# Kernel tuning notes

Measured on AMD Instinct MI355X. Metric: run time of the kernel, lower is better.

Reference implementation:

```python
import jax, jax.numpy as jnp
import numpy as np

D = 1024   # input_size / width
H = 1024   # hidden_size / lru_width
TW = 4     # conv1d temporal width (Griffin default)
C_GATE = 8.0


def setup_inputs() -> dict:
    key = jax.random.key(0)
    ks = jax.random.split(key, 12)
    B, T = 8, 4096
    sd = 1.0 / np.sqrt(D)
    sh = 1.0 / np.sqrt(H)
    return {
        "input_bxtxd": jax.random.normal(ks[0], (B, T, D), jnp.float32),
        "w_x": jax.random.normal(ks[1], (D, H), jnp.float32) * sd,
        "b_x": jnp.zeros((H,), jnp.float32),
        "w_y": jax.random.normal(ks[2], (D, H), jnp.float32) * sd,
        "b_y": jnp.zeros((H,), jnp.float32),
        "conv_w": jax.random.normal(ks[3], (TW, H), jnp.float32) * 0.5,
        "conv_b": jnp.zeros((H,), jnp.float32),
        "gi_w": jax.random.normal(ks[4], (H, H), jnp.float32) * sh,
        "gi_b": jnp.zeros((H,), jnp.float32),
        "ga_w": jax.random.normal(ks[5], (H, H), jnp.float32) * sh,
        "ga_b": jnp.zeros((H,), jnp.float32),
        # a_param > 0 so a = exp(-c*gate*softplus(a_param)) lies in (0,1)
        "a_param": jax.random.uniform(ks[6], (H,), jnp.float32, 2.0, 6.0),
    }


def reference(input_bxtxd, w_x, b_x, w_y, b_y, conv_w, conv_b,
              gi_w, gi_b, ga_w, ga_b, a_param):
    x = input_bxtxd                      # [B,T,D], batch_first
    B, T, _ = x.shape

    # x branch: linear_x -> causal depthwise conv1d (zero cache) -> RG-LRU
    x1 = jnp.einsum("btd,dh->bth", x, w_x) + b_x            # [B,T,H]
    xp = jnp.pad(x1, ((0, 0), (TW - 1, 0), (0, 0)))          # causal pad
    x2 = sum(conv_w[i] * xp[:, i:i + T, :] for i in range(TW)) + conv_b

    # RG-LRU gates (num_heads=1 -> full linear)
    gate_x = jax.nn.sigmoid(jnp.einsum("bth,hk->btk", x2, gi_w) + gi_b)
    gate_a = jax.nn.sigmoid(jnp.einsum("bth,hk->btk", x2, ga_w) + ga_b)
    log_a = -C_GATE * gate_a * jax.nn.softplus(a_param)      # [B,T,H]
    a = jnp.exp(log_a)
    multiplier = jnp.sqrt(jnp.maximum(1.0 - jnp.exp(2.0 * log_a), 0.0))
    # segment_pos = arange(T): reset at t == 0
    multiplier = multiplier.at[:, 0, :].set(1.0)
    a = a.at[:, 0, :].set(0.0)
    normalized_x = gate_x * x2 * multiplier                  # [B,T,H]

    # linear recurrence h_t = a_t * h_{t-1} + normalized_x_t (h_{-1}=0)
    def combine(c1, c2):
        a1, h1 = c1
        a2, h2 = c2
        return a1 * a2, h2 + a2 * h1

    _, h = jax.lax.associative_scan(combine, (a, normalized_x), axis=1)

    # y branch and output gating
    y = jax.nn.gelu(jnp.einsum("btd,dh->bth", x, w_y) + b_y, approximate=False)
    out = h * y                                              # [B,T,H]
    hn = h[:, -1, :]                                         # last state
    return out, h, hn
```

## Files before the change

### kernel.cpp

```cpp
#include <hip/hip_runtime.h>
#include <math.h>


#define B_ 8
#define T_ 4096
#define H_ 1024
#define M_ (B_ * T_)
#define NC_ 128
#define CL_ 32

typedef _Float16 half8 __attribute__((ext_vector_type(8)));
typedef _Float16 half4 __attribute__((ext_vector_type(4)));
typedef float    f32x4 __attribute__((ext_vector_type(4)));

#define FENCE asm volatile("" ::: "memory")
#define BAR() do { FENCE; __builtin_amdgcn_s_barrier(); FENCE; } while (0)
#define MFMA16(a, b, c) __builtin_amdgcn_mfma_f32_16x16x32_f16((a), (b), (c), 0, 0, 0)

__device__ __forceinline__ void load16_lds(const _Float16* g, _Float16* l) {
  __builtin_amdgcn_global_load_lds(
      (const __attribute__((address_space(1))) void*)g,
      (__attribute__((address_space(3))) void*)l, 16, 0, 0);
}

__global__ __launch_bounds__(256) void transpose_cvt(
    const float* __restrict__ sA, const float* __restrict__ sB,
    _Float16* __restrict__ dst) {
  __shared__ float tile[32][33];
  int bn = blockIdx.x * 32;
  int bk = blockIdx.y * 32;
  const float* src = (bn < 1024) ? sA : sB;
  int nof = (bn < 1024) ? bn : bn - 1024;
  int c  = threadIdx.x & 31;
  int r0 = threadIdx.x >> 5;
#pragma unroll
  for (int i = 0; i < 4; ++i) {
    int r = r0 + i * 8;
    tile[r][c] = src[(size_t)(bk + r) * 1024 + nof + c];
  }
  __syncthreads();
#pragma unroll
  for (int i = 0; i < 4; ++i) {
    int nl = r0 + i * 8;
    dst[(size_t)(bn + nl) * 1024 + bk + c] = (_Float16)tile[c][nl];
  }
}

__global__ void prep_bias(const float* __restrict__ bx, const float* __restrict__ by,
                          const float* __restrict__ gib, const float* __restrict__ gab,
                          float* __restrict__ b1, float* __restrict__ b2) {
  int i = blockIdx.x * 1024 + threadIdx.x;
  if (i < 1024)      b1[i] = bx[i];
  else if (i < 2048) b1[i] = by[i - 1024];
  else if (i < 3072) b2[i - 2048] = gib[i - 2048];
  else               b2[i - 2048] = gab[i - 3072];
}

__global__ __launch_bounds__(256) void cvt_fp16(
    const float* __restrict__ x, _Float16* __restrict__ xh, long n4) {
  for (long i = (long)blockIdx.x * 256 + threadIdx.x; i < n4;
       i += (long)gridDim.x * 256) {
    f32x4 v = ((const f32x4*)x)[i];
    half4 h;
#pragma unroll
    for (int e = 0; e < 4; ++e) h[e] = (_Float16)v[e];
    ((half4*)xh)[i] = h;
  }
}

template <int MODE>
__global__ __launch_bounds__(512, 2) void gemm_kernel(
    const _Float16* __restrict__ A, const _Float16* __restrict__ Bt,
    const float* __restrict__ bias, const float* __restrict__ a_param,
    _Float16* __restrict__ C) {
  __shared__ _Float16 ldsA[32768];
  __shared__ _Float16 ldsB[32768];
  int tid  = threadIdx.x;
  int lane = tid & 63;
  int wave = tid >> 6;
  int l15 = lane & 15, g = lane >> 4;

  int nb = ((int)blockIdx.x & 7) * 128 + ((int)blockIdx.x >> 3);
  int m0 = (nb >> 3) * 256;
  int n0 = (nb & 7) * 256;
  int wm = wave >> 2;
  int wn = wave & 3;

  int r0  = tid >> 3;
  int blk = (tid & 7) ^ (r0 & 7);
  const _Float16* pA = A  + (size_t)(m0 + r0) * 1024 + blk * 8;
  const _Float16* pB = Bt + (size_t)(n0 + r0) * 1024 + blk * 8;
  _Float16* stA = ldsA + wave * 512;
  _Float16* stB = ldsB + wave * 512;

#define STAGE_A(slot, mh, kt)                                                 \
  do {                                                                        \
    load16_lds(pA + (mh)*131072 + (kt)*64,         stA + (slot)*8192);        \
    load16_lds(pA + (mh)*131072 + 65536 + (kt)*64, stA + (slot)*8192 + 4096); \
  } while (0)
#define STAGE_B(slot, nu, kt)                                                 \
  do {                                                                        \
    load16_lds(pB + (nu)*131072 + (kt)*64,         stB + (slot)*8192);        \
    load16_lds(pB + (nu)*131072 + 65536 + (kt)*64, stB + (slot)*8192 + 4096); \
  } while (0)

  int xorf = (l15 & 7) << 3;
  int xa0 = (g * 8) ^ xorf;
  int xa1 = (32 + g * 8) ^ xorf;
  int aBase = l15 * 64;
  int bBase = ((wn & 1) * 64 + l15) * 64;
  int bUnit = wn >> 1;

  f32x4 acc[8][4];
#pragma unroll
  for (int i = 0; i < 8; ++i)
#pragma unroll
    for (int j = 0; j < 4; ++j) acc[i][j] = (f32x4){0.f, 0.f, 0.f, 0.f};

  STAGE_A(0, 0, 0); STAGE_A(1, 1, 0);
  STAGE_B(0, 0, 0); STAGE_B(1, 1, 0);
  asm volatile("s_waitcnt vmcnt(0)" ::: "memory");
  BAR();

  half8 a[8], b0, b1;
  for (int t = 0; t < 16; ++t) {
    int db = (t & 1) << 1;
    int dn = ((t + 1) & 1) << 1;
    int aS = (db + wm) * 8192 + aBase;
    int bS = (db + bUnit) * 8192 + bBase;
    bool pre = (t < 15);

#pragma unroll
    for (int mi = 0; mi < 8; ++mi)
      a[mi] = *(const half8*)(ldsA + aS + mi * 1024 + xa0);
    b0 = *(const half8*)(ldsB + bS + xa0);
    b1 = *(const half8*)(ldsB + bS + 1024 + xa0);
    if (pre) { STAGE_A(dn, 0, t + 1); STAGE_B(dn, 0, t + 1); }
    BAR();
    __builtin_amdgcn_s_setprio(1);
#pragma unroll
    for (int mi = 0; mi < 8; ++mi) acc[mi][0] = MFMA16(a[mi], b0, acc[mi][0]);
#pragma unroll
    for (int mi = 0; mi < 8; ++mi) acc[mi][1] = MFMA16(a[mi], b1, acc[mi][1]);
    __builtin_amdgcn_s_setprio(0);
    BAR();

    b0 = *(const half8*)(ldsB + bS + 2048 + xa0);
    b1 = *(const half8*)(ldsB + bS + 3072 + xa0);
    if (pre) { STAGE_A(dn + 1, 1, t + 1); STAGE_B(dn + 1, 1, t + 1); }
    BAR();
    __builtin_amdgcn_s_setprio(1);
#pragma unroll
    for (int mi = 0; mi < 8; ++mi) acc[mi][2] = MFMA16(a[mi], b0, acc[mi][2]);
#pragma unroll
    for (int mi = 0; mi < 8; ++mi) acc[mi][3] = MFMA16(a[mi], b1, acc[mi][3]);
    __builtin_amdgcn_s_setprio(0);
    BAR();

#pragma unroll
    for (int mi = 0; mi < 8; ++mi)
      a[mi] = *(const half8*)(ldsA + aS + mi * 1024 + xa1);
    b0 = *(const half8*)(ldsB + bS + xa1);
    b1 = *(const half8*)(ldsB + bS + 1024 + xa1);
    BAR();
    __builtin_amdgcn_s_setprio(1);
#pragma unroll
    for (int mi = 0; mi < 8; ++mi) acc[mi][0] = MFMA16(a[mi], b0, acc[mi][0]);
#pragma unroll
    for (int mi = 0; mi < 8; ++mi) acc[mi][1] = MFMA16(a[mi], b1, acc[mi][1]);
    __builtin_amdgcn_s_setprio(0);
    BAR();

    b0 = *(const half8*)(ldsB + bS + 2048 + xa1);
    b1 = *(const half8*)(ldsB + bS + 3072 + xa1);
    BAR();
    __builtin_amdgcn_s_setprio(1);
#pragma unroll
    for (int mi = 0; mi < 8; ++mi) acc[mi][2] = MFMA16(a[mi], b0, acc[mi][2]);
#pragma unroll
    for (int mi = 0; mi < 8; ++mi) acc[mi][3] = MFMA16(a[mi], b1, acc[mi][3]);
    __builtin_amdgcn_s_setprio(0);
    asm volatile("s_waitcnt vmcnt(0)" ::: "memory");
    BAR();
  }

  int   gn[4];
  float bs[4], sp[4];
#pragma unroll
  for (int nj = 0; nj < 4; ++nj) {
    gn[nj] = n0 + wn * 64 + nj * 16 + l15;
    bs[nj] = bias[gn[nj]];
    sp[nj] = 0.f;
    if (MODE == 1 && gn[nj] >= 1024)
      sp[nj] = log1pf(expf(a_param[gn[nj] - 1024]));
  }
#pragma unroll
  for (int mi = 0; mi < 8; ++mi) {
#pragma unroll
    for (int p = 0; p < 4; ++p) {
      int gm = m0 + wm * 128 + mi * 16 + g * 4 + p;
      size_t rowb = (size_t)gm * 2048;
#pragma unroll
      for (int nj = 0; nj < 4; ++nj) {
        float v = acc[mi][nj][p] + bs[nj];
        if (MODE == 1) {
          float s = 1.f / (1.f + expf(-v));
          if (gn[nj] < 1024) {
            v = s;
          } else {
            float av = expf(-8.f * s * sp[nj]);
            if ((gm & (T_ - 1)) == 0) av = 0.f;
            v = av;
          }
        }
        C[rowb + gn[nj]] = (_Float16)v;
      }
    }
  }
#undef STAGE_A
#undef STAGE_B
}

__global__ __launch_bounds__(256) void conv_kernel(
    const _Float16* __restrict__ g1, const float* __restrict__ cw,
    const float* __restrict__ cb, _Float16* __restrict__ x2) {
  int idx = blockIdx.x * 256 + threadIdx.x;
  int m  = idx >> 7;
  int hb = (idx & 127) * 8;
  int t  = m & (T_ - 1);
  float acc[8];
#pragma unroll
  for (int e = 0; e < 8; ++e) acc[e] = cb[hb + e];
#pragma unroll
  for (int j = 0; j < 4; ++j) {
    if (t >= j) {
      half8 xv = *(const half8*)&g1[(size_t)(m - j) * 2048 + hb];
      const float* w = &cw[(3 - j) * 1024 + hb];
#pragma unroll
      for (int e = 0; e < 8; ++e) acc[e] += w[e] * (float)xv[e];
    }
  }
  half8 o;
#pragma unroll
  for (int e = 0; e < 8; ++e) o[e] = (_Float16)acc[e];
  *(half8*)&x2[(size_t)m * 1024 + hb] = o;
}

__global__ __launch_bounds__(128) void scan1_kernel(
    const _Float16* __restrict__ g2, const _Float16* __restrict__ x2,
    float* __restrict__ cA, float* __restrict__ cH) {
  int bid = blockIdx.x;
  int b = bid >> 7, c = bid & 127;
  int h0 = threadIdx.x * 8;
  float A[8], Hh[8];
#pragma unroll
  for (int e = 0; e < 8; ++e) { A[e] = 1.f; Hh[e] = 0.f; }
  size_t mbase = (size_t)b * T_ + (size_t)c * CL_;
  for (int i = 0; i < CL_; ++i) {
    size_t m = mbase + i;
    half8 gx = *(const half8*)&g2[m * 2048 + h0];
    half8 av = *(const half8*)&g2[m * 2048 + 1024 + h0];
    half8 xv = *(const half8*)&x2[m * 1024 + h0];
#pragma unroll
    for (int e = 0; e < 8; ++e) {
      float a = (float)av[e];
      float mult = sqrtf(fmaxf(1.f - a * a, 0.f));
      float nx = (float)gx[e] * (float)xv[e] * mult;
      A[e] *= a;
      Hh[e] = nx + a * Hh[e];
    }
  }
  size_t o = (size_t)bid * 1024 + h0;
#pragma unroll
  for (int e = 0; e < 8; ++e) { cA[o + e] = A[e]; cH[o + e] = Hh[e]; }
}

__global__ void scanmid_kernel(const float* __restrict__ cA,
                               const float* __restrict__ cH,
                               float* __restrict__ carry) {
  int gidx = blockIdx.x * 256 + threadIdx.x;
  int b = gidx >> 10, h = gidx & 1023;
  float run = 0.f;
  for (int c = 0; c < NC_; ++c) {
    size_t o = ((size_t)(b * NC_ + c)) * 1024 + h;
    carry[o] = run;
    run = cH[o] + cA[o] * run;
  }
}

__global__ __launch_bounds__(128) void scan2_kernel(
    const _Float16* __restrict__ g2, const _Float16* __restrict__ x2,
    const _Float16* __restrict__ g1, const float* __restrict__ carry,
    float* __restrict__ outO, float* __restrict__ outH,
    float* __restrict__ outHn) {
  int bid = blockIdx.x;
  int b = bid >> 7, c = bid & 127;
  int h0 = threadIdx.x * 8;
  float Hh[8];
  {
    size_t o = (size_t)bid * 1024 + h0;
#pragma unroll
    for (int e = 0; e < 8; ++e) Hh[e] = carry[o + e];
  }
  size_t mbase = (size_t)b * T_ + (size_t)c * CL_;
  for (int i = 0; i < CL_; ++i) {
    size_t m = mbase + i;
    half8 gx = *(const half8*)&g2[m * 2048 + h0];
    half8 av = *(const half8*)&g2[m * 2048 + 1024 + h0];
    half8 xv = *(const half8*)&x2[m * 1024 + h0];
    half8 uv = *(const half8*)&g1[m * 2048 + 1024 + h0];
    f32x4 hO[2], oO[2];
#pragma unroll
    for (int e = 0; e < 8; ++e) {
      float a = (float)av[e];
      float mult = sqrtf(fmaxf(1.f - a * a, 0.f));
      float nx = (float)gx[e] * (float)xv[e] * mult;
      float v = nx + a * Hh[e];
      Hh[e] = v;
      float u = (float)uv[e];
      float y = 0.5f * u * (1.f + erff(u * 0.70710678118654752f));
      hO[e >> 2][e & 3] = v;
      oO[e >> 2][e & 3] = v * y;
    }
    size_t ob = m * 1024 + h0;
    *(f32x4*)&outH[ob]     = hO[0];
    *(f32x4*)&outH[ob + 4] = hO[1];
    *(f32x4*)&outO[ob]     = oO[0];
    *(f32x4*)&outO[ob + 4] = oO[1];
  }
  if (c == NC_ - 1) {
    size_t o = (size_t)b * 1024 + h0;
#pragma unroll
    for (int e = 0; e < 8; ++e) outHn[o + e] = Hh[e];
  }
}

extern "C" void kernel_launch(void* const* d_in, const int* in_sizes, int n_in,
                              void* d_out, int out_size, void* d_ws,
                              size_t ws_size, hipStream_t stream) {
  const float* x   = (const float*)d_in[0];
  const float* wx  = (const float*)d_in[1];
  const float* bx  = (const float*)d_in[2];
  const float* wy  = (const float*)d_in[3];
  const float* by  = (const float*)d_in[4];
  const float* cw  = (const float*)d_in[5];
  const float* cb  = (const float*)d_in[6];
  const float* giw = (const float*)d_in[7];
  const float* gib = (const float*)d_in[8];
  const float* gaw = (const float*)d_in[9];
  const float* gab = (const float*)d_in[10];
  const float* ap  = (const float*)d_in[11];

  char* ws = (char*)d_ws;
  size_t off = 0;
  auto alloc = [&](size_t bytes) {
    char* p = ws + off;
    off += (bytes + 255) & ~(size_t)255;
    return p;
  };
  _Float16* wT1 = (_Float16*)alloc((size_t)2048 * 1024 * 2);
  _Float16* wT2 = (_Float16*)alloc((size_t)2048 * 1024 * 2);
  float*    b1  = (float*)alloc(2048 * 4);
  float*    b2  = (float*)alloc(2048 * 4);
  _Float16* xh  = (_Float16*)alloc((size_t)M_ * 1024 * 2);
  _Float16* g2e = (_Float16*)alloc((size_t)M_ * 1024 * 2);
  (void)g2e;
  _Float16* g1o = (_Float16*)alloc((size_t)M_ * 2048 * 2);
  _Float16* x2h = (_Float16*)alloc((size_t)M_ * 1024 * 2);
  float* cA  = (float*)alloc((size_t)B_ * NC_ * 1024 * 4);
  float* cH  = (float*)alloc((size_t)B_ * NC_ * 1024 * 4);
  float* cin = (float*)alloc((size_t)B_ * NC_ * 1024 * 4);
  _Float16* g2o = xh;

  float* oO  = (float*)d_out;
  float* oH  = oO + (size_t)M_ * 1024;
  float* oHn = oO + (size_t)2 * M_ * 1024;

  transpose_cvt<<<dim3(64, 32), 256, 0, stream>>>(wx, wy, wT1);
  transpose_cvt<<<dim3(64, 32), 256, 0, stream>>>(giw, gaw, wT2);
  prep_bias<<<4, 1024, 0, stream>>>(bx, by, gib, gab, b1, b2);
  cvt_fp16<<<2048, 256, 0, stream>>>(x, xh, (long)M_ * 1024 / 4);

  gemm_kernel<0><<<1024, 512, 0, stream>>>(xh, wT1, b1, nullptr, g1o);
  conv_kernel<<<16384, 256, 0, stream>>>(g1o, cw, cb, x2h);
  gemm_kernel<1><<<1024, 512, 0, stream>>>(x2h, wT2, b2, ap, g2o);

  scan1_kernel<<<B_ * NC_, 128, 0, stream>>>(g2o, x2h, cA, cH);
  scanmid_kernel<<<32, 256, 0, stream>>>(cA, cH, cin);
  scan2_kernel<<<B_ * NC_, 128, 0, stream>>>(g2o, x2h, g1o, cin, oO, oH, oHn);
}
```

Before: 620.0 us.

## Restructure GEMM main loop with deeper prefetch and partial vmcnt waits

Rewrites the GEMM k-loop staging. Global-to-LDS loads are now split into k-halves and issued up to two k-tiles ahead. The full vmcnt(0) drain each iteration is replaced by partial vmcnt waits, with explicit peeled tail iterations. It also changes the LDS layout and XOR swizzle for the A and B fragments and reorders MFMA issue so each wave works on 4x4 sub-blocks at a time. The aim is to hide global load latency behind MFMA work, at the cost of fragile wait counts that must match the number of in-flight loads exactly.

```diff
diff --git a/kernel.cpp b/kernel.cpp
--- a/kernel.cpp
+++ b/kernel.cpp
@@ -16,6 +16,10 @@
 #define FENCE asm volatile("" ::: "memory")
 #define BAR() do { FENCE; __builtin_amdgcn_s_barrier(); FENCE; } while (0)
 #define MFMA16(a, b, c) __builtin_amdgcn_mfma_f32_16x16x32_f16((a), (b), (c), 0, 0, 0)
+#define VM10 asm volatile("s_waitcnt vmcnt(10)" ::: "memory")
+#define VM8  asm volatile("s_waitcnt vmcnt(8)"  ::: "memory")
+#define VM4  asm volatile("s_waitcnt vmcnt(4)"  ::: "memory")
+#define VM0  asm volatile("s_waitcnt vmcnt(0)"  ::: "memory")
 
 __device__ __forceinline__ void load16_lds(const _Float16* g, _Float16* l) {
   __builtin_amdgcn_global_load_lds(
@@ -86,30 +90,30 @@
   int wm = wave >> 2;
   int wn = wave & 3;
 
-  int r0  = tid >> 3;
-  int blk = (tid & 7) ^ (r0 & 7);
-  const _Float16* pA = A  + (size_t)(m0 + r0) * 1024 + blk * 8;
-  const _Float16* pB = Bt + (size_t)(n0 + r0) * 1024 + blk * 8;
+  int gsrc = (tid & 3) ^ ((tid >> 3) & 3);
+  const _Float16* pA = A  + (size_t)(m0 + (tid >> 2)) * 1024 + gsrc * 8;
+  const _Float16* pB = Bt + (size_t)(n0 + (tid >> 2)) * 1024 + gsrc * 8;
   _Float16* stA = ldsA + wave * 512;
   _Float16* stB = ldsB + wave * 512;
 
-#define STAGE_A(slot, mh, kt)                                                 \
+#define STAGE_A(kt, kh)                                                       \
   do {                                                                        \
-    load16_lds(pA + (mh)*131072 + (kt)*64,         stA + (slot)*8192);        \
-    load16_lds(pA + (mh)*131072 + 65536 + (kt)*64, stA + (slot)*8192 + 4096); \
+    const _Float16* s_ = pA + (kt) * 64 + (kh) * 32;                          \
+    _Float16* d_ = stA + (((kt) & 1) * 2 + (kh)) * 8192;                      \
+    load16_lds(s_, d_);                                    \
+    load16_lds(s_ + 131072, d_ + 4096);                    \
   } while (0)
-#define STAGE_B(slot, nu, kt)                                                 \
+#define STAGE_B(kt, kh)                                                       \
   do {                                                                        \
-    load16_lds(pB + (nu)*131072 + (kt)*64,         stB + (slot)*8192);        \
-    load16_lds(pB + (nu)*131072 + 65536 + (kt)*64, stB + (slot)*8192 + 4096); \
+    const _Float16* s_ = pB + (kt) * 64 + (kh) * 32;                          \
+    _Float16* d_ = stB + (((kt) & 1) * 2 + (kh)) * 8192;                      \
+    load16_lds(s_, d_);                                                       \
+    load16_lds(s_ + 131072, d_ + 4096);                                       \
   } while (0)
 
-  int xorf = (l15 & 7) << 3;
-  int xa0 = (g * 8) ^ xorf;
-  int xa1 = (32 + g * 8) ^ xorf;
-  int aBase = l15 * 64;
-  int bBase = ((wn & 1) * 64 + l15) * 64;
-  int bUnit = wn >> 1;
+  int jj8  = ((g ^ ((l15 >> 1) & 3)) << 3);
+  int aoff = wm * 4096 + l15 * 32 + jj8;
+  int boff = wn * 2048 + l15 * 32 + jj8;
 
   f32x4 acc[8][4];
 #pragma unroll
@@ -117,72 +121,88 @@
 #pragma unroll
     for (int j = 0; j < 4; ++j) acc[i][j] = (f32x4){0.f, 0.f, 0.f, 0.f};
 
-  STAGE_A(0, 0, 0); STAGE_A(1, 1, 0);
-  STAGE_B(0, 0, 0); STAGE_B(1, 1, 0);
-  asm volatile("s_waitcnt vmcnt(0)" ::: "memory");
+  half8 a0[4], a1[4], b[4];
+
+#define KTILE(SL, ST0, ST1, ST2, ST3, W1, W2)                                 \
+  do {                                                                        \
+    const int pl = (SL) * 16384;                                              \
+                                               \
+    _Pragma("unroll") for (int q = 0; q < 4; ++q)                             \
+      a0[q] = *(const half8*)(ldsA + pl + q * 512 + aoff);                    \
+    _Pragma("unroll") for (int q = 0; q < 4; ++q)                             \
+      b[q]  = *(const half8*)(ldsB + pl + q * 512 + boff);                    \
+    ST0;                                                                      \
+    BAR();                                                                    \
+    __builtin_amdgcn_s_setprio(1);                                            \
+    _Pragma("unroll") for (int q = 0; q < 4; ++q) {                           \
+      acc[q][0] = MFMA16(a0[q], b[0], acc[q][0]);                             \
+      acc[q][1] = MFMA16(a0[q], b[1], acc[q][1]);                             \
+      acc[q][2] = MFMA16(a0[q], b[2], acc[q][2]);                             \
+      acc[q][3] = MFMA16(a0[q], b[3], acc[q][3]);                             \
+    }                                                                         \
+    __builtin_amdgcn_s_setprio(0);                                            \
+    BAR();                                                                    \
+                                               \
+    _Pragma("unroll") for (int q = 0; q < 4; ++q)                             \
+      a1[q] = *(const half8*)(ldsA + pl + 2048 + q * 512 + aoff);             \
+    ST1;                                                                      \
+    BAR();                                                                    \
+    __builtin_amdgcn_s_setprio(1);                                            \
+    _Pragma("unroll") for (int q = 0; q < 4; ++q) {                           \
+      acc[4 + q][0] = MFMA16(a1[q], b[0], acc[4 + q][0]);                     \
+      acc[4 + q][1] = MFMA16(a1[q], b[1], acc[4 + q][1]);                     \
+      acc[4 + q][2] = MFMA16(a1[q], b[2], acc[4 + q][2]);                     \
+      acc[4 + q][3] = MFMA16(a1[q], b[3], acc[4 + q][3]);                     \
+    }                                                                         \
+    __builtin_amdgcn_s_setprio(0);                                            \
+    W1;                                                                       \
+    BAR();                                                                    \
+                                               \
+    _Pragma("unroll") for (int q = 0; q < 4; ++q)                             \
+      a0[q] = *(const half8*)(ldsA + pl + 8192 + q * 512 + aoff);             \
+    _Pragma("unroll") for (int q = 0; q < 4; ++q)                             \
+      b[q]  = *(const half8*)(ldsB + pl + 8192 + q * 512 + boff);             \
+    ST2;                                                                      \
+    BAR();                                                                    \
+    __builtin_amdgcn_s_setprio(1);                                            \
+    _Pragma("unroll") for (int q = 0; q < 4; ++q) {                           \
+      acc[q][0] = MFMA16(a0[q], b[0], acc[q][0]);                             \
+      acc[q][1] = MFMA16(a0[q], b[1], acc[q][1]);                             \
+      acc[q][2] = MFMA16(a0[q], b[2], acc[q][2]);                             \
+      acc[q][3] = MFMA16(a0[q], b[3], acc[q][3]);                             \
+    }                                                                         \
+    __builtin_amdgcn_s_setprio(0);                                            \
+    BAR();                                                                    \
+                                               \
+    _Pragma("unroll") for (int q = 0; q < 4; ++q)                             \
+      a1[q] = *(const half8*)(ldsA + pl + 8192 + 2048 + q * 512 + aoff);      \
+    ST3;                                                                      \
+    BAR();                                                                    \
+    __builtin_amdgcn_s_setprio(1);                                            \
+    _Pragma("unroll") for (int q = 0; q < 4; ++q) {                           \
+      acc[4 + q][0] = MFMA16(a1[q], b[0], acc[4 + q][0]);                     \
+      acc[4 + q][1] = MFMA16(a1[q], b[1], acc[4 + q][1]);                     \
+      acc[4 + q][2] = MFMA16(a1[q], b[2], acc[4 + q][2]);                     \
+      acc[4 + q][3] = MFMA16(a1[q], b[3], acc[4 + q][3]);                     \
+    }                                                                         \
+    __builtin_amdgcn_s_setprio(0);                                            \
+    W2;                                                                       \
+    BAR();                                                                    \
+  } while (0)
+
+  STAGE_B(0, 0); STAGE_A(0, 0); STAGE_B(0, 1); STAGE_A(0, 1);
+  STAGE_B(1, 0); STAGE_A(1, 0); STAGE_B(1, 1);
+  VM10;
   BAR();
 
-  half8 a[8], b0, b1;
-  for (int t = 0; t < 16; ++t) {
-    int db = (t & 1) << 1;
-    int dn = ((t + 1) & 1) << 1;
-    int aS = (db + wm) * 8192 + aBase;
-    int bS = (db + bUnit) * 8192 + bBase;
-    bool pre = (t < 15);
-
-#pragma unroll
-    for (int mi = 0; mi < 8; ++mi)
-      a[mi] = *(const half8*)(ldsA + aS + mi * 1024 + xa0);
-    b0 = *(const half8*)(ldsB + bS + xa0);
-    b1 = *(const half8*)(ldsB + bS + 1024 + xa0);
-    if (pre) { STAGE_A(dn, 0, t + 1); STAGE_B(dn, 0, t + 1); }
-    BAR();
-    __builtin_amdgcn_s_setprio(1);
-#pragma unroll
-    for (int mi = 0; mi < 8; ++mi) acc[mi][0] = MFMA16(a[mi], b0, acc[mi][0]);
-#pragma unroll
-    for (int mi = 0; mi < 8; ++mi) acc[mi][1] = MFMA16(a[mi], b1, acc[mi][1]);
-    __builtin_amdgcn_s_setprio(0);
-    BAR();
-
-    b0 = *(const half8*)(ldsB + bS + 2048 + xa0);
-    b1 = *(const half8*)(ldsB + bS + 3072 + xa0);
-    if (pre) { STAGE_A(dn + 1, 1, t + 1); STAGE_B(dn + 1, 1, t + 1); }
-    BAR();
-    __builtin_amdgcn_s_setprio(1);
-#pragma unroll
-    for (int mi = 0; mi < 8; ++mi) acc[mi][2] = MFMA16(a[mi], b0, acc[mi][2]);
-#pragma unroll
-    for (int mi = 0; mi < 8; ++mi) acc[mi][3] = MFMA16(a[mi], b1, acc[mi][3]);
-    __builtin_amdgcn_s_setprio(0);
-    BAR();
-
-#pragma unroll
-    for (int mi = 0; mi < 8; ++mi)
-      a[mi] = *(const half8*)(ldsA + aS + mi * 1024 + xa1);
-    b0 = *(const half8*)(ldsB + bS + xa1);
-    b1 = *(const half8*)(ldsB + bS + 1024 + xa1);
-    BAR();
-    __builtin_amdgcn_s_setprio(1);
-#pragma unroll
-    for (int mi = 0; mi < 8; ++mi) acc[mi][0] = MFMA16(a[mi], b0, acc[mi][0]);
-#pragma unroll
-    for (int mi = 0; mi < 8; ++mi) acc[mi][1] = MFMA16(a[mi], b1, acc[mi][1]);
-    __builtin_amdgcn_s_setprio(0);
-    BAR();
-
-    b0 = *(const half8*)(ldsB + bS + 2048 + xa1);
-    b1 = *(const half8*)(ldsB + bS + 3072 + xa1);
-    BAR();
-    __builtin_amdgcn_s_setprio(1);
-#pragma unroll
-    for (int mi = 0; mi < 8; ++mi) acc[mi][2] = MFMA16(a[mi], b0, acc[mi][2]);
-#pragma unroll
-    for (int mi = 0; mi < 8; ++mi) acc[mi][3] = MFMA16(a[mi], b1, acc[mi][3]);
-    __builtin_amdgcn_s_setprio(0);
-    asm volatile("s_waitcnt vmcnt(0)" ::: "memory");
-    BAR();
-  }
+  for (int t = 0; t < 14; ++t) {
+    KTILE((t & 1),
+          STAGE_A(t + 1, 1), STAGE_B(t + 2, 0),
+          STAGE_A(t + 2, 0), STAGE_B(t + 2, 1),
+          VM10, VM10);
+  }
+  KTILE(0, STAGE_A(15, 1), (void)0, (void)0, (void)0, VM8, VM4);
+  KTILE(1, (void)0, (void)0, (void)0, (void)0, VM0, (void)0);
 
   int   gn[4];
   float bs[4], sp[4];
@@ -219,6 +239,7 @@
   }
 #undef STAGE_A
 #undef STAGE_B
+#undef KTILE
 }
 
 __global__ __launch_bounds__(256) void conv_kernel(
```

Result: no change. 628.5 us (+1.4%).
